# Performance work log

Hardware: AMD Instinct MI355X
Metric: run time of the kernel (lower is better)

Reference implementation:

```python
import jax, jax.numpy as jnp
import numpy as np

B, C_IN, N = 2048, 128, 128
M = N - 1  # conv output positions per tree (stride-3 kernel-3 over 3*M gathered triples)


def setup_inputs() -> dict:
    key = jax.random.key(0)
    ks = jax.random.split(key, 8)
    trees = jax.random.normal(ks[0], (B, C_IN, N), jnp.float32)
    trees = trees.at[:, :, 0].set(0.0)  # slot 0 is the zero-pad node
    indexes = jax.random.randint(ks[1], (B, 3 * M), 0, N)

    def wconv(k, o, c):
        return jax.random.normal(k, (o, c, 3), jnp.float32) * 0.05

    return {
        "trees": trees,
        "indexes": indexes,
        "W1": wconv(ks[2], 256, C_IN), "b1": jnp.zeros((256,), jnp.float32),
        "W2": wconv(ks[3], 128, 256), "b2": jnp.zeros((128,), jnp.float32),
        "W3": wconv(ks[4], 64, 128), "b3": jnp.zeros((64,), jnp.float32),
        "W4": jax.random.normal(ks[5], (32, 64), jnp.float32) * 0.1,
        "b4": jnp.zeros((32,), jnp.float32),
        "W5": jax.random.normal(ks[6], (1, 32), jnp.float32) * 0.1,
        "b5": jnp.zeros((1,), jnp.float32),
    }


def _tree_conv(data, idx, W, b):
    # data: [B, C, N]; idx: [B, 3M] of (self, left, right) node indices
    g = jnp.take_along_axis(data, idx[:, None, :], axis=2)        # [B, C, 3M] gather
    g = g.reshape(data.shape[0], data.shape[1], -1, 3)            # [B, C, M, 3]
    out = jnp.einsum('bcmk,ock->bom', g, W) + b[None, :, None]    # Conv1d(k=3, s=3)
    zero = jnp.zeros((out.shape[0], out.shape[1], 1), out.dtype)  # re-prepend zero slot
    return jnp.concatenate([zero, out], axis=2)                   # [B, O, N]


def _tree_layer_norm(data):
    # normalize over (channels, nodes) per tree; torch.std is unbiased (ddof=1)
    mean = jnp.mean(data, axis=(1, 2), keepdims=True)
    std = jnp.std(data, axis=(1, 2), keepdims=True, ddof=1)
    return (data - mean) / (std + 1e-5)


def _leaky(x):
    return jax.nn.leaky_relu(x, 0.01)


def reference(trees, W1, b1, W2, b2, W3, b3, W4, b4, W5, b5, indexes):
    x = _leaky(_tree_layer_norm(_tree_conv(trees, indexes, W1, b1)))
    x = _leaky(_tree_layer_norm(_tree_conv(x, indexes, W2, b2)))
    x = _tree_layer_norm(_tree_conv(x, indexes, W3, b3))
    pooled = jnp.max(x, axis=2)                                   # DynamicPooling -> [B, 64]
    h = _leaky(pooled @ W4.T + b4)
    return h @ W5.T + b5                                          # [B, 1]
```

## Files before the change

kernel.cpp:

```cpp
#include <hip/hip_runtime.h>

typedef unsigned short u16;
typedef __attribute__((ext_vector_type(8)))  short          short8;
typedef __attribute__((ext_vector_type(8)))  unsigned short ushort8v;
typedef __attribute__((ext_vector_type(4)))  unsigned short ushort4v;
typedef __attribute__((ext_vector_type(16))) float          float16v;

__device__ __forceinline__ float bf2f(u16 u){
  union { unsigned int i; float f; } x; x.i = ((unsigned int)u) << 16; return x.f;
}
__device__ __forceinline__ u16 f2bf(float f){
  union { float f; unsigned int i; } x; x.f = f;
  unsigned int u = x.i;
  unsigned int r = (u + 0x7FFFu + ((u >> 16) & 1u)) >> 16;
  return (u16)r;
}
__device__ __forceinline__ float lk(float v){ return v > 0.f ? v : 0.01f*v; }

__global__ void permute_w(const float* __restrict__ W1, const float* __restrict__ W2,
                          const float* __restrict__ W3, u16* __restrict__ ws){
  int t = blockIdx.x*256 + threadIdx.x;
  const float* src; u16* dst; int C, local;
  if (t < 98304)       { src = W1; dst = ws;          C = 128; local = t; }
  else if (t < 196608) { src = W2; dst = ws + 98304;  C = 256; local = t - 98304; }
  else if (t < 221184) { src = W3; dst = ws + 196608; C = 128; local = t - 196608; }
  else return;
  const int NJK  = 3*C/16;
  const int tile = local >> 9, within = local & 511;
  const int lane = within >> 3, e = within & 7;
  const int rb = tile / NJK, jk = tile - rb*NJK;
  const int o  = rb*32 + (lane & 31);
  const int kg = jk*16 + (lane >> 5)*8 + e;
  const int j  = kg / C, c = kg - j*C;
  dst[local] = f2bf(src[o*3*C + c*3 + j]);
}

template<int CIN, int O, int SIN, int OST, int NTL, bool LEAKY, bool IS_L3>
__device__ __forceinline__ void do_layer(const u16* __restrict__ Wt,
                                         const float* __restrict__ bias,
                                         const u16* bIn, u16* bOut, float* bOutF,
                                         const int* sidx, float* sstat,
                                         int tid, float* out_mean, float* out_inv)
{
  constexpr int KS  = CIN/16;
  constexpr int NJK = 3*KS;
  static_assert((O/64)*4 == 4*NTL, "work split mismatch");
  const int w = tid >> 6, lane = tid & 63, l31 = lane & 31, h = lane >> 5;

  const int u0  = w*NTL;
  const int rb  = u0 >> 2;
  const int nt0 = u0 & 3;
  const int r0  = rb * 64;

  const u16* aP[2] = { Wt + ((size_t)(rb*2    )*NJK)*512 + lane*8,
                       Wt + ((size_t)(rb*2 + 1)*NJK)*512 + lane*8 };

  int boff[NTL][3];
#pragma unroll
  for (int n = 0; n < NTL; ++n){
    int m = (nt0 + n)*32 + l31;
#pragma unroll
    for (int j = 0; j < 3; ++j){
      int i = sidx[3*m + j];
      boff[n][j] = i*SIN + h*8;
    }
  }

  float16v acc[NTL][2];
#pragma unroll
  for (int n = 0; n < NTL; ++n){ acc[n][0] = {}; acc[n][1] = {}; }

#pragma unroll
  for (int jk = 0; jk < NJK; ++jk){
    const int j    = jk / KS;
    const int coff = (jk - j*KS)*16;
    short8 A0 = *(const short8*)(aP[0] + jk*512);
    short8 A1 = *(const short8*)(aP[1] + jk*512);
#pragma unroll
    for (int n = 0; n < NTL; ++n){
      short8 Bf = *(const short8*)(bIn + boff[n][j] + coff);
      acc[n][0] = __builtin_amdgcn_mfma_f32_32x32x16_bf16(A0, Bf, acc[n][0], 0, 0, 0);
      acc[n][1] = __builtin_amdgcn_mfma_f32_32x32x16_bf16(A1, Bf, acc[n][1], 0, 0, 0);
    }
  }

  float s = 0.f, s2 = 0.f;
#pragma unroll
  for (int n = 0; n < NTL; ++n){
    const int m = (nt0 + n)*32 + l31;
    const bool valid = (m <= 126);
#pragma unroll
    for (int a = 0; a < 2; ++a)
#pragma unroll
      for (int g = 0; g < 4; ++g){
        const int rowb = r0 + a*32 + 8*g + 4*h;
#pragma unroll
        for (int q = 0; q < 4; ++q){
          float raw = acc[n][a][4*g + q] + bias[rowb + q];
          acc[n][a][4*g + q] = raw;
          if (valid){ s += raw; s2 += raw*raw; }
        }
      }
  }

#pragma unroll
  for (int off = 32; off >= 1; off >>= 1){
    s  += __shfl_down(s,  off, 64);
    s2 += __shfl_down(s2, off, 64);
  }
  if (lane == 0){ sstat[w*2] = s; sstat[w*2+1] = s2; }
  __syncthreads();

  const float tot  = sstat[0] + sstat[2] + sstat[4] + sstat[6];
  const float tot2 = sstat[1] + sstat[3] + sstat[5] + sstat[7];
  constexpr float CNT = (float)(O * 128);
  const float mean = tot / CNT;
  float var = (tot2 - tot*mean) / (CNT - 1.f);
  var = fmaxf(var, 0.f);
  const float inv = 1.f / (sqrtf(var) + 1e-5f);
  *out_mean = mean; *out_inv = inv;

  if constexpr (!IS_L3){
#pragma unroll
    for (int n = 0; n < NTL; ++n){
      const int m = (nt0 + n)*32 + l31;
      const bool valid = (m <= 126);
#pragma unroll
      for (int a = 0; a < 2; ++a){
#pragma unroll
        for (int g = 0; g < 4; ++g){
          const int rowb = r0 + a*32 + 8*g + 4*h;
          ushort4v pk;
#pragma unroll
          for (int q = 0; q < 4; ++q){
            float f = (acc[n][a][4*g + q] - mean) * inv;
            if constexpr (LEAKY) f = lk(f);
            pk[q] = f2bf(f);
          }
          if (valid) *(ushort4v*)(bOut + (size_t)(m+1)*OST + rowb) = pk;
        }
      }
    }
    if (tid < O/8){
      float f0 = (0.f - mean) * inv;
      if constexpr (LEAKY) f0 = lk(f0);
      const u16 v0 = f2bf(f0);
      ushort8v z;
#pragma unroll
      for (int e = 0; e < 8; ++e) z[e] = v0;
      *(ushort8v*)(bOut + tid*8) = z;
    }
  } else {
#pragma unroll
    for (int n = 0; n < NTL; ++n){
      const int m = (nt0 + n)*32 + l31;
      if (m <= 126){
#pragma unroll
        for (int a = 0; a < 2; ++a)
#pragma unroll
          for (int g = 0; g < 4; ++g){
            const int rowb = r0 + a*32 + 8*g + 4*h;
#pragma unroll
            for (int q = 0; q < 4; ++q)
              bOutF[(size_t)(m+1)*OST + rowb + q] = acc[n][a][4*g + q];
          }
      }
    }
  }
  __syncthreads();
}

__global__ __launch_bounds__(256, 2) void bao_main(
    const float* __restrict__ trees, const int* __restrict__ gidx,
    const u16* __restrict__ wsW,
    const float* __restrict__ b1, const float* __restrict__ b2, const float* __restrict__ b3,
    const float* __restrict__ W4, const float* __restrict__ b4,
    const float* __restrict__ W5, const float* __restrict__ b5,
    float* __restrict__ dout)
{
  __shared__ __align__(16) u16 buf[33792];
  __shared__ int   sidx[384];
  __shared__ float sstat[8];
  __shared__ float spoolP[256];
  __shared__ float spool[64];
  __shared__ float sh[32];

  const int tid = threadIdx.x;
  const int b = blockIdx.x;
  float* bufF = (float*)buf;

  const float* tb = trees + (size_t)b * (128*128);
  {
    const int ngrp = tid & 31, cg = tid >> 5;
#pragma unroll
    for (int it = 0; it < 8; ++it){
      const int n  = ngrp + 32*(it & 3);
      const int c0 = (cg + 8*(it >> 2))*8;
      ushort8v pk;
#pragma unroll
      for (int cc = 0; cc < 8; ++cc) pk[cc] = f2bf(tb[(c0 + cc)*128 + n]);
      *(ushort8v*)(buf + n*136 + c0) = pk;
    }
  }
  if (tid < 96){
#pragma unroll
    for (int k = 0; k < 4; ++k){
      int ii = tid*4 + k;
      sidx[ii] = (ii < 381) ? gidx[(size_t)b*381 + ii] : 0;
    }
  }
  __syncthreads();

  float mean, inv;
  do_layer<128,256,136,264, 4, true ,false>(wsW,          b1, buf, buf, nullptr, sidx, sstat, tid, &mean, &inv);
  do_layer<256,128,264,136, 2, true ,false>(wsW + 98304,  b2, buf, buf, nullptr, sidx, sstat, tid, &mean, &inv);
  do_layer<128, 64,136, 67, 1, false,true >(wsW + 196608, b3, buf, nullptr, bufF, sidx, sstat, tid, &mean, &inv);

  {
    const int ch = tid & 63, seg = tid >> 6;
    float mx = 0.f;
    const int nd0 = seg*32 + (seg == 0 ? 1 : 0);
    for (int nd = nd0; nd < seg*32 + 32; ++nd) mx = fmaxf(mx, bufF[nd*67 + ch]);
    spoolP[seg*64 + ch] = mx;
  }
  __syncthreads();
  if (tid < 64){
    float mx = fmaxf(fmaxf(spoolP[tid], spoolP[64 + tid]),
                     fmaxf(spoolP[128 + tid], spoolP[192 + tid]));
    spool[tid] = (mx - mean) * inv;
  }
  __syncthreads();
  if (tid < 32){
    float a = b4[tid];
    for (int c = 0; c < 64; ++c) a += spool[c] * W4[tid*64 + c];
    sh[tid] = lk(a);
  }
  __syncthreads();
  if (tid == 0){
    float o = b5[0];
    for (int i = 0; i < 32; ++i) o += sh[i] * W5[i];
    dout[b] = o;
  }
}

extern "C" void kernel_launch(void* const* d_in, const int* in_sizes, int n_in,
                              void* d_out, int out_size, void* d_ws, size_t ws_size,
                              hipStream_t stream) {
  const float* trees = (const float*)d_in[0];
  const int*   gidx  = (const int*)d_in[1];
  const float* W1 = (const float*)d_in[2];
  const float* b1 = (const float*)d_in[3];
  const float* W2 = (const float*)d_in[4];
  const float* b2 = (const float*)d_in[5];
  const float* W3 = (const float*)d_in[6];
  const float* b3 = (const float*)d_in[7];
  const float* W4 = (const float*)d_in[8];
  const float* b4 = (const float*)d_in[9];
  const float* W5 = (const float*)d_in[10];
  const float* b5 = (const float*)d_in[11];
  u16* wsW = (u16*)d_ws;

  permute_w<<<864, 256, 0, stream>>>(W1, W2, W3, wsW);
  bao_main<<<2048, 256, 0, stream>>>(trees, gidx, wsW, b1, b2, b3, W4, b4, W5, b5,
                                     (float*)d_out);
}
```

Baseline: 333.7 us.

## Double workgroup to 512 threads, splitting per-layer MFMA tiles across eight waves

Each per-tree workgroup grows from 4 to 8 wavefronts. Layers 1 and 2 split their MFMA output tiles over all eight waves, while layer 3 keeps four active waves and the rest idle. Input staging, pooling and the stats reduction are rewritten for the larger thread count, and launch bounds now target 4 waves per SIMD. The intent is more latency hiding and more MFMA issue parallelism per tree, at the cost of fewer accumulators per wave, idle waves in layer 3, and tighter register limits under the new launch bounds.

```diff
diff --git a/kernel.cpp b/kernel.cpp
--- a/kernel.cpp
+++ b/kernel.cpp
@@ -35,7 +35,7 @@
   dst[local] = f2bf(src[o*3*C + c*3 + j]);
 }
 
-template<int CIN, int O, int SIN, int OST, int NTL, bool LEAKY, bool IS_L3>
+template<int CIN, int O, int SIN, int OST, int NTL, int NACT, bool LEAKY, bool IS_L3>
 __device__ __forceinline__ void do_layer(const u16* __restrict__ Wt,
                                          const float* __restrict__ bias,
                                          const u16* bIn, u16* bOut, float* bOutF,
@@ -44,10 +44,12 @@
 {
   constexpr int KS  = CIN/16;
   constexpr int NJK = 3*KS;
-  static_assert((O/64)*4 == 4*NTL, "work split mismatch");
+  static_assert((O/64)*4 == NACT*NTL, "work split mismatch");
   const int w = tid >> 6, lane = tid & 63, l31 = lane & 31, h = lane >> 5;
-
-  const int u0  = w*NTL;
+  const bool active = (w < NACT);
+  const int wa = active ? w : 0;
+
+  const int u0  = wa*NTL;
   const int rb  = u0 >> 2;
   const int nt0 = u0 & 3;
   const int r0  = rb * 64;
@@ -55,52 +57,55 @@
   const u16* aP[2] = { Wt + ((size_t)(rb*2    )*NJK)*512 + lane*8,
                        Wt + ((size_t)(rb*2 + 1)*NJK)*512 + lane*8 };
 
-  int boff[NTL][3];
-#pragma unroll
-  for (int n = 0; n < NTL; ++n){
-    int m = (nt0 + n)*32 + l31;
-#pragma unroll
-    for (int j = 0; j < 3; ++j){
-      int i = sidx[3*m + j];
-      boff[n][j] = i*SIN + h*8;
-    }
-  }
-
   float16v acc[NTL][2];
-#pragma unroll
-  for (int n = 0; n < NTL; ++n){ acc[n][0] = {}; acc[n][1] = {}; }
-
-#pragma unroll
-  for (int jk = 0; jk < NJK; ++jk){
-    const int j    = jk / KS;
-    const int coff = (jk - j*KS)*16;
-    short8 A0 = *(const short8*)(aP[0] + jk*512);
-    short8 A1 = *(const short8*)(aP[1] + jk*512);
+  float s = 0.f, s2 = 0.f;
+
+  if (active){
+    int boff[NTL][3];
 #pragma unroll
     for (int n = 0; n < NTL; ++n){
-      short8 Bf = *(const short8*)(bIn + boff[n][j] + coff);
-      acc[n][0] = __builtin_amdgcn_mfma_f32_32x32x16_bf16(A0, Bf, acc[n][0], 0, 0, 0);
-      acc[n][1] = __builtin_amdgcn_mfma_f32_32x32x16_bf16(A1, Bf, acc[n][1], 0, 0, 0);
-    }
-  }
-
-  float s = 0.f, s2 = 0.f;
-#pragma unroll
-  for (int n = 0; n < NTL; ++n){
-    const int m = (nt0 + n)*32 + l31;
-    const bool valid = (m <= 126);
-#pragma unroll
-    for (int a = 0; a < 2; ++a)
-#pragma unroll
-      for (int g = 0; g < 4; ++g){
-        const int rowb = r0 + a*32 + 8*g + 4*h;
-#pragma unroll
-        for (int q = 0; q < 4; ++q){
-          float raw = acc[n][a][4*g + q] + bias[rowb + q];
-          acc[n][a][4*g + q] = raw;
-          if (valid){ s += raw; s2 += raw*raw; }
+      int m = (nt0 + n)*32 + l31;
+#pragma unroll
+      for (int j = 0; j < 3; ++j){
+        int i = sidx[3*m + j];
+        boff[n][j] = i*SIN + h*8;
+      }
+    }
+
+#pragma unroll
+    for (int n = 0; n < NTL; ++n){ acc[n][0] = {}; acc[n][1] = {}; }
+
+#pragma unroll
+    for (int jk = 0; jk < NJK; ++jk){
+      const int j    = jk / KS;
+      const int coff = (jk - j*KS)*16;
+      short8 A0 = *(const short8*)(aP[0] + jk*512);
+      short8 A1 = *(const short8*)(aP[1] + jk*512);
+#pragma unroll
+      for (int n = 0; n < NTL; ++n){
+        short8 Bf = *(const short8*)(bIn + boff[n][j] + coff);
+        acc[n][0] = __builtin_amdgcn_mfma_f32_32x32x16_bf16(A0, Bf, acc[n][0], 0, 0, 0);
+        acc[n][1] = __builtin_amdgcn_mfma_f32_32x32x16_bf16(A1, Bf, acc[n][1], 0, 0, 0);
+      }
+    }
+
+#pragma unroll
+    for (int n = 0; n < NTL; ++n){
+      const int m = (nt0 + n)*32 + l31;
+      const bool valid = (m <= 126);
+#pragma unroll
+      for (int a = 0; a < 2; ++a)
+#pragma unroll
+        for (int g = 0; g < 4; ++g){
+          const int rowb = r0 + a*32 + 8*g + 4*h;
+#pragma unroll
+          for (int q = 0; q < 4; ++q){
+            float raw = acc[n][a][4*g + q] + bias[rowb + q];
+            acc[n][a][4*g + q] = raw;
+            if (valid){ s += raw; s2 += raw*raw; }
+          }
         }
-      }
+    }
   }
 
 #pragma unroll
@@ -111,8 +116,9 @@
   if (lane == 0){ sstat[w*2] = s; sstat[w*2+1] = s2; }
   __syncthreads();
 
-  const float tot  = sstat[0] + sstat[2] + sstat[4] + sstat[6];
-  const float tot2 = sstat[1] + sstat[3] + sstat[5] + sstat[7];
+  float tot = 0.f, tot2 = 0.f;
+#pragma unroll
+  for (int q = 0; q < 8; ++q){ tot += sstat[2*q]; tot2 += sstat[2*q+1]; }
   constexpr float CNT = (float)(O * 128);
   const float mean = tot / CNT;
   float var = (tot2 - tot*mean) / (CNT - 1.f);
@@ -121,23 +127,25 @@
   *out_mean = mean; *out_inv = inv;
 
   if constexpr (!IS_L3){
-#pragma unroll
-    for (int n = 0; n < NTL; ++n){
-      const int m = (nt0 + n)*32 + l31;
-      const bool valid = (m <= 126);
-#pragma unroll
-      for (int a = 0; a < 2; ++a){
-#pragma unroll
-        for (int g = 0; g < 4; ++g){
-          const int rowb = r0 + a*32 + 8*g + 4*h;
-          ushort4v pk;
-#pragma unroll
-          for (int q = 0; q < 4; ++q){
-            float f = (acc[n][a][4*g + q] - mean) * inv;
-            if constexpr (LEAKY) f = lk(f);
-            pk[q] = f2bf(f);
+    if (active){
+#pragma unroll
+      for (int n = 0; n < NTL; ++n){
+        const int m = (nt0 + n)*32 + l31;
+        const bool valid = (m <= 126);
+#pragma unroll
+        for (int a = 0; a < 2; ++a){
+#pragma unroll
+          for (int g = 0; g < 4; ++g){
+            const int rowb = r0 + a*32 + 8*g + 4*h;
+            ushort4v pk;
+#pragma unroll
+            for (int q = 0; q < 4; ++q){
+              float f = (acc[n][a][4*g + q] - mean) * inv;
+              if constexpr (LEAKY) f = lk(f);
+              pk[q] = f2bf(f);
+            }
+            if (valid) *(ushort4v*)(bOut + (size_t)(m+1)*OST + rowb) = pk;
           }
-          if (valid) *(ushort4v*)(bOut + (size_t)(m+1)*OST + rowb) = pk;
         }
       }
     }
@@ -151,26 +159,28 @@
       *(ushort8v*)(bOut + tid*8) = z;
     }
   } else {
-#pragma unroll
-    for (int n = 0; n < NTL; ++n){
-      const int m = (nt0 + n)*32 + l31;
-      if (m <= 126){
-#pragma unroll
-        for (int a = 0; a < 2; ++a)
-#pragma unroll
-          for (int g = 0; g < 4; ++g){
-            const int rowb = r0 + a*32 + 8*g + 4*h;
-#pragma unroll
-            for (int q = 0; q < 4; ++q)
-              bOutF[(size_t)(m+1)*OST + rowb + q] = acc[n][a][4*g + q];
-          }
-      }
-    }
-  }
-  __syncthreads();
-}
-
-__global__ __launch_bounds__(256, 2) void bao_main(
+    if (active){
+#pragma unroll
+      for (int n = 0; n < NTL; ++n){
+        const int m = (nt0 + n)*32 + l31;
+        if (m <= 126){
+#pragma unroll
+          for (int a = 0; a < 2; ++a)
+#pragma unroll
+            for (int g = 0; g < 4; ++g){
+              const int rowb = r0 + a*32 + 8*g + 4*h;
+#pragma unroll
+              for (int q = 0; q < 4; ++q)
+                bOutF[(size_t)(m+1)*OST + rowb + q] = acc[n][a][4*g + q];
+            }
+        }
+      }
+    }
+  }
+  __syncthreads();
+}
+
+__global__ __launch_bounds__(512, 4) void bao_main(
     const float* __restrict__ trees, const int* __restrict__ gidx,
     const u16* __restrict__ wsW,
     const float* __restrict__ b1, const float* __restrict__ b2, const float* __restrict__ b3,
@@ -180,8 +190,8 @@
 {
   __shared__ __align__(16) u16 buf[33792];
   __shared__ int   sidx[384];
-  __shared__ float sstat[8];
-  __shared__ float spoolP[256];
+  __shared__ float sstat[16];
+  __shared__ float spoolP[512];
   __shared__ float spool[64];
   __shared__ float sh[32];
 
@@ -192,10 +202,10 @@
   const float* tb = trees + (size_t)b * (128*128);
   {
     const int ngrp = tid & 31, cg = tid >> 5;
-#pragma unroll
-    for (int it = 0; it < 8; ++it){
-      const int n  = ngrp + 32*(it & 3);
-      const int c0 = (cg + 8*(it >> 2))*8;
+    const int c0 = cg*8;
+#pragma unroll
+    for (int it = 0; it < 4; ++it){
+      const int n = ngrp + 32*it;
       ushort8v pk;
 #pragma unroll
       for (int cc = 0; cc < 8; ++cc) pk[cc] = f2bf(tb[(c0 + cc)*128 + n]);
@@ -212,21 +222,22 @@
   __syncthreads();
 
   float mean, inv;
-  do_layer<128,256,136,264, 4, true ,false>(wsW,          b1, buf, buf, nullptr, sidx, sstat, tid, &mean, &inv);
-  do_layer<256,128,264,136, 2, true ,false>(wsW + 98304,  b2, buf, buf, nullptr, sidx, sstat, tid, &mean, &inv);
-  do_layer<128, 64,136, 67, 1, false,true >(wsW + 196608, b3, buf, nullptr, bufF, sidx, sstat, tid, &mean, &inv);
+  do_layer<128,256,136,264, 2, 8, true ,false>(wsW,          b1, buf, buf, nullptr, sidx, sstat, tid, &mean, &inv);
+  do_layer<256,128,264,136, 1, 8, true ,false>(wsW + 98304,  b2, buf, buf, nullptr, sidx, sstat, tid, &mean, &inv);
+  do_layer<128, 64,136, 67, 1, 4, false,true >(wsW + 196608, b3, buf, nullptr, bufF, sidx, sstat, tid, &mean, &inv);
 
   {
     const int ch = tid & 63, seg = tid >> 6;
     float mx = 0.f;
-    const int nd0 = seg*32 + (seg == 0 ? 1 : 0);
-    for (int nd = nd0; nd < seg*32 + 32; ++nd) mx = fmaxf(mx, bufF[nd*67 + ch]);
+    const int nd0 = seg*16 + (seg == 0 ? 1 : 0);
+    for (int nd = nd0; nd < seg*16 + 16; ++nd) mx = fmaxf(mx, bufF[nd*67 + ch]);
     spoolP[seg*64 + ch] = mx;
   }
   __syncthreads();
   if (tid < 64){
-    float mx = fmaxf(fmaxf(spoolP[tid], spoolP[64 + tid]),
-                     fmaxf(spoolP[128 + tid], spoolP[192 + tid]));
+    float mx = spoolP[tid];
+#pragma unroll
+    for (int k = 1; k < 8; ++k) mx = fmaxf(mx, spoolP[64*k + tid]);
     spool[tid] = (mx - mean) * inv;
   }
   __syncthreads();
@@ -261,6 +272,6 @@
   u16* wsW = (u16*)d_ws;
 
   permute_w<<<864, 256, 0, stream>>>(W1, W2, W3, wsW);
-  bao_main<<<2048, 256, 0, stream>>>(trees, gidx, wsW, b1, b2, b3, W4, b4, W5, b5,
+  bao_main<<<2048, 512, 0, stream>>>(trees, gidx, wsW, b1, b2, b3, W4, b4, W5, b5,
                                      (float*)d_out);
 }
```

Measured after the change: 346.4 us. 1.04x slower.
